# Kernel tuning notes

Measured on AMD Instinct MI355X. Metric: run time of the kernel, lower is better.

The kernel has to match this reference:

```python
import jax, jax.numpy as jnp
import numpy as np

STRIDE = (1, 1)
PADDING = ((1, 1), (1, 1))


def setup_inputs() -> dict:
    key = jax.random.key(0)
    kx, kw, kb = jax.random.split(key, 3)
    x = jax.random.normal(kx, (32, 128, 56, 56), dtype=jnp.float32)
    weight = jax.random.normal(kw, (256, 128, 3, 3), dtype=jnp.float32)  # (O, I, kh, kw)
    bias = jax.random.normal(kb, (256,), dtype=jnp.float32)
    return {"x": x, "weight": weight, "bias": bias}


def reference(x, weight, bias):
    # Faithful dense 2D convolution (cross-correlation, as in the torch module),
    # NCHW input, OIHW weight, stride 1, padding 1.
    out = jax.lax.conv_general_dilated(
        x, weight,
        window_strides=STRIDE,
        padding=PADDING,
        dimension_numbers=("NCHW", "OIHW", "NCHW"),
    )
    return out + bias[None, :, None, None]
```

## Files before the change

### kernel.cpp

```cpp
#include <hip/hip_runtime.h>

#define C_IN   128
#define H_IN   56
#define W_IN   56
#define HW     3136
#define CHW    401408
#define O_OUT  256
#define OHW    802816

#define LDK 72
#define XTP 132

typedef __bf16 bf16x8 __attribute__((ext_vector_type(8)));
typedef float  f32x4  __attribute__((ext_vector_type(4)));
typedef unsigned short ushort_t;
typedef ushort_t ushort8 __attribute__((ext_vector_type(8)));

__device__ __forceinline__ ushort_t f2bf(float f) {
    union { float f; unsigned u; } v; v.f = f;
    unsigned r = (v.u + 0x7fffu + ((v.u >> 16) & 1u)) >> 16;
    return (ushort_t)r;
}

typedef const __attribute__((address_space(1))) unsigned int* gas_ptr;
typedef __attribute__((address_space(3))) unsigned int* las_ptr;
__device__ __forceinline__ void gl_lds16(const void* g, void* l) {
    __builtin_amdgcn_global_load_lds((gas_ptr)g, (las_ptr)l, 16, 0, 0);
}


__global__ void wt2_kernel(const float* __restrict__ w, ushort_t* __restrict__ wbf) {
    int idx = blockIdx.x * 256 + threadIdx.x;
    if (idx >= 9 * 256 * 128) return;
    int pos = idx >> 15;
    int rem = idx & 32767;
    int o   = rem >> 7;
    int c   = rem & 127;
    int s    = pos * 2 + (c >> 6);
    int slot = ((c >> 3) & 7) ^ (o & 7);
    wbf[((s * 256 + o) << 6) + (slot << 3) + (c & 7)] = f2bf(w[o * 1152 + c * 9 + pos]);
}

__global__ __launch_bounds__(256)
void xt2_kernel(const float* __restrict__ x, ushort_t* __restrict__ xbp) {
    const int b  = blockIdx.x;
    const int n  = b / 58;
    const int hp = b - n * 58;
    ushort_t* orow = xbp + (size_t)(n * 58 + hp) * 7424;
    const int t = threadIdx.x;
    ushort8 z = ushort8{0,0,0,0,0,0,0,0};

    if (hp == 0 || hp == 57) {
        #pragma unroll
        for (int i = 0; i < 4; ++i) {
            int u = i * 256 + t;
            if (u < 928) *(ushort8*)(orow + u * 8) = z;
        }
        return;
    }

    __shared__ ushort_t T[56 * XTP];
    const int h = hp - 1;
    const float* src = x + (size_t)n * CHW + h * W_IN;
    #pragma unroll
    for (int i = 0; i < 7; ++i) {
        int g  = i * 256 + t;
        int c  = g / 14;
        int f4 = g - c * 14;
        f32x4 v = *(const f32x4*)(src + (size_t)c * HW + f4 * 4);
        #pragma unroll
        for (int j = 0; j < 4; ++j)
            T[(f4 * 4 + j) * XTP + c] = f2bf(v[j]);
    }
    __syncthreads();
    #pragma unroll
    for (int i = 0; i < 4; ++i) {
        int u = i * 256 + t;
        if (u < 928) {
            int wp = u >> 4, gg = u & 15;
            ushort8 v = (wp == 0 || wp == 57) ? z
                        : *(const ushort8*)(&T[(wp - 1) * XTP + gg * 8]);
            *(ushort8*)(orow + wp * 128 + ((gg ^ (wp & 7)) << 3)) = v;
        }
    }
}

__global__ __launch_bounds__(256, 3)
void conv12_kernel(const ushort_t* __restrict__ xbp, const ushort_t* __restrict__ wbf,
                   const float* __restrict__ bias, float* __restrict__ out) {
    __shared__ ushort_t As[128 * 64];
    __shared__ ushort_t Bs[128 * 64];

    const int tid  = threadIdx.x;
    const int lane = tid & 63;
    const int wave = tid >> 6;
    const int wm   = wave >> 1;
    const int wn   = wave & 1;
    const int l15  = lane & 15;
    const int quad = lane >> 4;
    const int om   = wm * 64;

    int tau = blockIdx.x;
    tau = (tau & 7) * 196 + (tau >> 3);
    const int pix_base = (tau >> 1) * 128;
    const int ob       = (tau & 1) << 7;

    long Bc[4];
    {
        #pragma unroll
        for (int c = 0; c < 4; ++c) {
            int idx = (wave * 4 + c) * 64 + lane;
            int px  = idx >> 3;
            int j8  = idx & 7;
            int p   = pix_base + px;
            int n_  = p / HW;
            int hw  = p - n_ * HW;
            int h   = hw / W_IN;
            int w_  = hw - h * W_IN;
            Bc[c] = (long)(n_ * 58 + h + 1) * 14848 + (long)(w_ + 1) * 256 + j8 * 16;
        }
    }

    int aoff[4];
    #pragma unroll
    for (int t = 0; t < 4; ++t) {
        int ol = om + t * 16 + l15;
        aoff[t] = ol * 128 + ((quad ^ (ol & 7)) << 4);
    }
    int pxb[4], pr7[4], obo[4];
    #pragma unroll
    for (int u = 0; u < 4; ++u) {
        int pxr = wn * 64 + u * 16 + l15;
        int p   = pix_base + pxr;
        pxb[u]  = pxr * 128;
        pr7[u]  = (p + 1) & 7;
        obo[u]  = p;
    }

    f32x4 acc[4][4];
    #pragma unroll
    for (int t = 0; t < 4; ++t)
        #pragma unroll
        for (int u = 0; u < 4; ++u)
            acc[t][u] = f32x4{0.f, 0.f, 0.f, 0.f};

    const char* xg = (const char*)xbp;
    const char* wg = (const char*)wbf;
    char* AsB = (char*)As;
    char* BsB = (char*)Bs;

    for (int q = 0; q < 18; ++q) {
        const int pos  = q >> 1;
        const int half = q & 1;
        const int dh   = pos / 3 - 1;
        const int dw   = pos - (pos / 3) * 3 - 1;
        const long soff = (long)dh * 14848 + (long)dw * 256 + half * 128;

        {
            const char* as = wg + (size_t)q * 32768 + (size_t)ob * 128;
            #pragma unroll
            for (int j = 0; j < 4; ++j) {
                const int blk = (wave * 4 + j) * 1024;
                gl_lds16(as + blk + (lane << 4), AsB + blk);
                gl_lds16(xg + Bc[j] + soff,      BsB + blk);
            }
        }
        __syncthreads();

        int boff[4];
        #pragma unroll
        for (int u = 0; u < 4; ++u) {
            const int key = (pr7[u] + dw + 8) & 7;
            boff[u] = pxb[u] + ((quad ^ key) << 4);
        }
        #pragma unroll
        for (int ks = 0; ks < 2; ++ks) {
            const int kx = ks << 6;
            bf16x8 af[4], bf[4];
            #pragma unroll
            for (int t = 0; t < 4; ++t)
                af[t] = *(const bf16x8*)(AsB + (aoff[t] ^ kx));
            #pragma unroll
            for (int u = 0; u < 4; ++u)
                bf[u] = *(const bf16x8*)(BsB + (boff[u] ^ kx));
            #pragma unroll
            for (int t = 0; t < 4; ++t)
                #pragma unroll
                for (int u = 0; u < 4; ++u)
                    acc[t][u] = __builtin_amdgcn_mfma_f32_16x16x32_bf16(
                                    af[t], bf[u], acc[t][u], 0, 0, 0);
        }
        __syncthreads();
    }

    #pragma unroll
    for (int u = 0; u < 4; ++u) {
        const int pp  = obo[u];
        const int nn  = pp / HW;
        const int hw2 = pp - nn * HW;
        const long obase = (long)nn * OHW + hw2;
        #pragma unroll
        for (int t = 0; t < 4; ++t) {
            const int o_base = ob + wm * 64 + t * 16 + quad * 4;
            #pragma unroll
            for (int r = 0; r < 4; ++r) {
                const int o = o_base + r;
                out[obase + (long)o * HW] = acc[t][u][r] + bias[o];
            }
        }
    }
}


__global__ void wt_kernel(const float* __restrict__ w, ushort_t* __restrict__ wbf) {
    int idx = blockIdx.x * 256 + threadIdx.x;
    if (idx >= 9 * 256 * 128) return;
    int pos = idx >> 15;
    int rem = idx & 32767;
    int o   = rem >> 7;
    int c   = rem & 127;
    wbf[idx] = f2bf(w[o * 1152 + c * 9 + pos]);
}

__global__ __launch_bounds__(512, 4)
void conv_kernel(const float* __restrict__ x, const ushort_t* __restrict__ wbf,
                 const float* __restrict__ bias, float* __restrict__ out) {
    __shared__ ushort_t As[256 * LDK];
    __shared__ ushort_t Bs[128 * LDK];

    const int tid  = threadIdx.x;
    const int lane = tid & 63;
    const int wave = tid >> 6;
    const int wm   = wave >> 1;
    const int wn   = wave & 1;
    const int l15  = lane & 15;
    const int quad = lane >> 4;

    const int pix_base = blockIdx.x * 128;
    const int px  = tid & 127;
    const int cg0 = tid >> 7;
    const int p   = pix_base + px;
    const int n_img = p / HW;
    const int hw    = p - n_img * HW;
    const int h     = hw / W_IN;
    const int w_    = hw - h * W_IN;
    const float* ximg = x + (long)n_img * CHW;

    f32x4 acc[4][4];
    #pragma unroll
    for (int t = 0; t < 4; ++t)
        #pragma unroll
        for (int u = 0; u < 4; ++u)
            acc[t][u] = f32x4{0.f, 0.f, 0.f, 0.f};

    for (int pos = 0; pos < 9; ++pos) {
        const int dh = pos / 3 - 1;
        const int dw = pos - (pos / 3) * 3 - 1;
        const int ih = h + dh;
        const int iw = w_ + dw;
        const bool valid = ((unsigned)ih < (unsigned)H_IN) && ((unsigned)iw < (unsigned)W_IN);
        const float* xsrc = ximg + ih * W_IN + iw;

        for (int half = 0; half < 2; ++half) {
            const int c0 = half * 64;
            {
                const ushort_t* wsrc = wbf + ((pos * 256) << 7) + c0;
                #pragma unroll
                for (int sj = 0; sj < 4; ++sj) {
                    const int o  = (tid >> 3) + sj * 64;
                    const int cg = tid & 7;
                    ushort8 v = *(const ushort8*)(wsrc + (o << 7) + cg * 8);
                    *(ushort8*)(&As[o * LDK + cg * 8]) = v;
                }
            }
            {
                #pragma unroll
                for (int sj = 0; sj < 2; ++sj) {
                    const int cg = cg0 + sj * 4;
                    const float* src = xsrc + (long)(c0 + cg * 8) * HW;
                    ushort8 v;
                    #pragma unroll
                    for (int j = 0; j < 8; ++j) {
                        float f = valid ? src[j * HW] : 0.0f;
                        v[j] = f2bf(f);
                    }
                    *(ushort8*)(&Bs[px * LDK + cg * 8]) = v;
                }
            }
            __syncthreads();

            #pragma unroll
            for (int ks = 0; ks < 2; ++ks) {
                bf16x8 af[4], bfv[4];
                #pragma unroll
                for (int t = 0; t < 4; ++t) {
                    const int row = wm * 64 + t * 16 + l15;
                    af[t] = *(const bf16x8*)(&As[row * LDK + ks * 32 + quad * 8]);
                }
                #pragma unroll
                for (int u = 0; u < 4; ++u) {
                    const int col = wn * 64 + u * 16 + l15;
                    bfv[u] = *(const bf16x8*)(&Bs[col * LDK + ks * 32 + quad * 8]);
                }
                #pragma unroll
                for (int t = 0; t < 4; ++t)
                    #pragma unroll
                    for (int u = 0; u < 4; ++u)
                        acc[t][u] = __builtin_amdgcn_mfma_f32_16x16x32_bf16(af[t], bfv[u], acc[t][u], 0, 0, 0);
            }
            __syncthreads();
        }
    }

    #pragma unroll
    for (int u = 0; u < 4; ++u) {
        const int col = wn * 64 + u * 16 + l15;
        const int pp  = pix_base + col;
        const int hw2 = pp - (pp / HW) * HW;
        const long obase = (long)(pp / HW) * OHW + hw2;
        #pragma unroll
        for (int t = 0; t < 4; ++t) {
            const int o_base = wm * 64 + t * 16 + quad * 4;
            #pragma unroll
            for (int r = 0; r < 4; ++r) {
                const int o = o_base + r;
                out[obase + (long)o * HW] = acc[t][u][r] + bias[o];
            }
        }
    }
}

extern "C" void kernel_launch(void* const* d_in, const int* in_sizes, int n_in,
                              void* d_out, int out_size, void* d_ws, size_t ws_size,
                              hipStream_t stream) {
    const float* x    = (const float*)d_in[0];
    const float* w    = (const float*)d_in[1];
    const float* bias = (const float*)d_in[2];
    float* out        = (float*)d_out;

    const size_t NEED_NEW = 589824u + 27557888u;

    if (ws_size >= NEED_NEW) {
        ushort_t* wbf = (ushort_t*)d_ws;
        ushort_t* xbp = (ushort_t*)((char*)d_ws + 589824);
        hipLaunchKernelGGL(wt2_kernel, dim3(1152), dim3(256), 0, stream, w, wbf);
        hipLaunchKernelGGL(xt2_kernel, dim3(1856), dim3(256), 0, stream, x, xbp);
        hipLaunchKernelGGL(conv12_kernel, dim3(1568), dim3(256), 0, stream,
                           xbp, wbf, bias, out);
    } else {
        ushort_t* wbf = (ushort_t*)d_ws;
        hipLaunchKernelGGL(wt_kernel, dim3(1152), dim3(256), 0, stream, w, wbf);
        hipLaunchKernelGGL(conv_kernel, dim3(100352 / 128), dim3(512), 0, stream,
                           x, wbf, bias, out);
    }
}
```

Baseline: 209.6 us.

## Triple-buffer LDS with 32-wide K steps and full 256-channel output tiles

```diff
diff --git a/kernel.cpp b/kernel.cpp
--- a/kernel.cpp
+++ b/kernel.cpp
@@ -29,20 +29,24 @@
 }
 
 
-__global__ void wt2_kernel(const float* __restrict__ w, ushort_t* __restrict__ wbf) {
+__global__ void wt5_kernel(const float* __restrict__ w, ushort_t* __restrict__ wbf) {
     int idx = blockIdx.x * 256 + threadIdx.x;
-    if (idx >= 9 * 256 * 128) return;
-    int pos = idx >> 15;
-    int rem = idx & 32767;
-    int o   = rem >> 7;
-    int c   = rem & 127;
-    int s    = pos * 2 + (c >> 6);
-    int slot = ((c >> 3) & 7) ^ (o & 7);
-    wbf[((s * 256 + o) << 6) + (slot << 3) + (c & 7)] = f2bf(w[o * 1152 + c * 9 + pos]);
+    if (idx >= 294912) return;
+    int v  = idx >> 13;
+    int r  = idx & 8191;
+    int o  = r >> 5;
+    int s  = r & 31;
+    int j2 = s >> 3;
+    int e  = s & 7;
+    int a   = v & 3;
+    int pos = v >> 2;
+    int g2 = j2 ^ ((o >> 1) & 3);
+    int c  = a * 32 + g2 * 8 + e;
+    wbf[idx] = f2bf(w[o * 1152 + c * 9 + pos]);
 }
 
 __global__ __launch_bounds__(256)
-void xt2_kernel(const float* __restrict__ x, ushort_t* __restrict__ xbp) {
+void xt3_kernel(const float* __restrict__ x, ushort_t* __restrict__ xbp) {
     const int b  = blockIdx.x;
     const int n  = b / 58;
     const int hp = b - n * 58;
@@ -80,16 +84,19 @@
             int wp = u >> 4, gg = u & 15;
             ushort8 v = (wp == 0 || wp == 57) ? z
                         : *(const ushort8*)(&T[(wp - 1) * XTP + gg * 8]);
-            *(ushort8*)(orow + wp * 128 + ((gg ^ (wp & 7)) << 3)) = v;
-        }
-    }
-}
-
-__global__ __launch_bounds__(256, 3)
-void conv12_kernel(const ushort_t* __restrict__ xbp, const ushort_t* __restrict__ wbf,
+            const int a  = gg >> 2;
+            const int g2 = gg & 3;
+            const int k  = (wp & 3) ^ ((wp >> 2) & 3);
+            *(ushort8*)(orow + wp * 128 + ((a * 4 + (g2 ^ k)) << 3)) = v;
+        }
+    }
+}
+
+__global__ __launch_bounds__(512, 4)
+void conv13_kernel(const ushort_t* __restrict__ xbp, const ushort_t* __restrict__ wbf,
                    const float* __restrict__ bias, float* __restrict__ out) {
-    __shared__ ushort_t As[128 * 64];
-    __shared__ ushort_t Bs[128 * 64];
+    __shared__ ushort_t Alds[3][8192];
+    __shared__ ushort_t Blds[3][4096];
 
     const int tid  = threadIdx.x;
     const int lane = tid & 63;
@@ -98,43 +105,42 @@
     const int wn   = wave & 1;
     const int l15  = lane & 15;
     const int quad = lane >> 4;
-    const int om   = wm * 64;
-
-    int tau = blockIdx.x;
-    tau = (tau & 7) * 196 + (tau >> 3);
-    const int pix_base = (tau >> 1) * 128;
-    const int ob       = (tau & 1) << 7;
-
-    long Bc[4];
+    const int wb10 = wave << 10;
+
+    int b = blockIdx.x;
+    b = (b & 7) * 98 + (b >> 3);
+    const int pix_base = b * 128;
+
+    int aoff[4];
+    #pragma unroll
+    for (int t = 0; t < 4; ++t) {
+        int o = wm * 64 + t * 16 + l15;
+        aoff[t] = o * 64 + ((quad ^ ((o >> 1) & 3)) << 4);
+    }
+
+    int pxb[4], w1[4];
+    #pragma unroll
+    for (int u = 0; u < 4; ++u) {
+        int px = wn * 64 + u * 16 + l15;
+        int p  = pix_base + px;
+        int n_ = p / HW;
+        int hw = p - n_ * HW;
+        int h  = hw / W_IN;
+        int w_ = hw - h * W_IN;
+        pxb[u] = px * 64;
+        w1[u]  = w_ + 1;
+    }
+
+    int Brow;
     {
-        #pragma unroll
-        for (int c = 0; c < 4; ++c) {
-            int idx = (wave * 4 + c) * 64 + lane;
-            int px  = idx >> 3;
-            int j8  = idx & 7;
-            int p   = pix_base + px;
-            int n_  = p / HW;
-            int hw  = p - n_ * HW;
-            int h   = hw / W_IN;
-            int w_  = hw - h * W_IN;
-            Bc[c] = (long)(n_ * 58 + h + 1) * 14848 + (long)(w_ + 1) * 256 + j8 * 16;
-        }
-    }
-
-    int aoff[4];
-    #pragma unroll
-    for (int t = 0; t < 4; ++t) {
-        int ol = om + t * 16 + l15;
-        aoff[t] = ol * 128 + ((quad ^ (ol & 7)) << 4);
-    }
-    int pxb[4], pr7[4], obo[4];
-    #pragma unroll
-    for (int u = 0; u < 4; ++u) {
-        int pxr = wn * 64 + u * 16 + l15;
-        int p   = pix_base + pxr;
-        pxb[u]  = pxr * 128;
-        pr7[u]  = (p + 1) & 7;
-        obo[u]  = p;
+        int spx = tid >> 2;
+        int j2  = tid & 3;
+        int sp  = pix_base + spx;
+        int sn  = sp / HW;
+        int shw = sp - sn * HW;
+        int sh  = shw / W_IN;
+        int sw  = shw - sh * W_IN;
+        Brow = ((sn * 58 + sh + 1) * 58 + (sw + 1)) * 256 + j2 * 16;
     }
 
     f32x4 acc[4][4];
@@ -144,69 +150,84 @@
         for (int u = 0; u < 4; ++u)
             acc[t][u] = f32x4{0.f, 0.f, 0.f, 0.f};
 
-    const char* xg = (const char*)xbp;
-    const char* wg = (const char*)wbf;
-    char* AsB = (char*)As;
-    char* BsB = (char*)Bs;
-
-    for (int q = 0; q < 18; ++q) {
-        const int pos  = q >> 1;
-        const int half = q & 1;
-        const int dh   = pos / 3 - 1;
-        const int dw   = pos - (pos / 3) * 3 - 1;
-        const long soff = (long)dh * 14848 + (long)dw * 256 + half * 128;
-
-        {
-            const char* as = wg + (size_t)q * 32768 + (size_t)ob * 128;
-            #pragma unroll
-            for (int j = 0; j < 4; ++j) {
-                const int blk = (wave * 4 + j) * 1024;
-                gl_lds16(as + blk + (lane << 4), AsB + blk);
-                gl_lds16(xg + Bc[j] + soff,      BsB + blk);
-            }
-        }
-        __syncthreads();
-
-        int boff[4];
+    const char* wgb = (const char*)wbf;
+    const char* xgb = (const char*)xbp;
+
+    char* A0 = (char*)Alds[0]; char* A1 = (char*)Alds[1]; char* A2 = (char*)Alds[2];
+    char* B0 = (char*)Blds[0]; char* B1 = (char*)Blds[1]; char* B2 = (char*)Blds[2];
+
+#define ISSUE(vv, Ad, Bd) { \
+    const int v_ = (vv); \
+    const int pos_ = v_ >> 2, a_ = v_ & 3; \
+    const int dh_ = pos_ / 3 - 1; \
+    const int dw_ = pos_ - (pos_ / 3) * 3 - 1; \
+    const char* as_ = wgb + (size_t)v_ * 16384; \
+    gl_lds16(as_ + wb10 + (lane << 4),        (Ad) + wb10); \
+    gl_lds16(as_ + 8192 + wb10 + (lane << 4), (Ad) + 8192 + wb10); \
+    const int soff_ = (dh_ * 58 + dw_) * 256 + a_ * 64; \
+    gl_lds16(xgb + (long)(Brow + soff_),      (Bd) + wb10); }
+
+    ISSUE(0, A0, B0);
+    ISSUE(1, A1, B1);
+    asm volatile("s_waitcnt vmcnt(3)" ::: "memory");
+    __builtin_amdgcn_s_barrier();
+
+    for (int q = 0; q < 36; ++q) {
+        const int pos = q >> 2;
+        const int dw  = pos - (pos / 3) * 3 - 1;
+
+        bf16x8 af[4], bf[4];
+        #pragma unroll
+        for (int t = 0; t < 4; ++t)
+            af[t] = *(const bf16x8*)(A0 + aoff[t]);
         #pragma unroll
         for (int u = 0; u < 4; ++u) {
-            const int key = (pr7[u] + dw + 8) & 7;
-            boff[u] = pxb[u] + ((quad ^ key) << 4);
-        }
-        #pragma unroll
-        for (int ks = 0; ks < 2; ++ks) {
-            const int kx = ks << 6;
-            bf16x8 af[4], bf[4];
-            #pragma unroll
-            for (int t = 0; t < 4; ++t)
-                af[t] = *(const bf16x8*)(AsB + (aoff[t] ^ kx));
+            const int ww  = w1[u] + dw;
+            const int key = (ww & 3) ^ ((ww >> 2) & 3);
+            bf[u] = *(const bf16x8*)(B0 + pxb[u] + ((quad ^ key) << 4));
+        }
+
+        if (q < 34) ISSUE(q + 2, A2, B2);
+
+        __builtin_amdgcn_s_barrier();
+        asm volatile("s_waitcnt lgkmcnt(0)" ::: "memory");
+        __builtin_amdgcn_sched_barrier(0);
+        __builtin_amdgcn_s_setprio(1);
+        #pragma unroll
+        for (int t = 0; t < 4; ++t)
             #pragma unroll
             for (int u = 0; u < 4; ++u)
-                bf[u] = *(const bf16x8*)(BsB + (boff[u] ^ kx));
+                acc[t][u] = __builtin_amdgcn_mfma_f32_16x16x32_bf16(
+                                af[t], bf[u], acc[t][u], 0, 0, 0);
+        __builtin_amdgcn_s_setprio(0);
+        __builtin_amdgcn_sched_barrier(0);
+
+        if (q < 34) asm volatile("s_waitcnt vmcnt(3)" ::: "memory");
+        else        asm volatile("s_waitcnt vmcnt(0)" ::: "memory");
+        __builtin_amdgcn_s_barrier();
+
+        char* tA = A0; A0 = A1; A1 = A2; A2 = tA;
+        char* tB = B0; B0 = B1; B1 = B2; B2 = tB;
+    }
+#undef ISSUE
+
+    f32x4 bv[4];
+    #pragma unroll
+    for (int t = 0; t < 4; ++t)
+        bv[t] = *(const f32x4*)(bias + wm * 64 + t * 16 + quad * 4);
+    #pragma unroll
+    for (int u = 0; u < 4; ++u) {
+        const int px  = wn * 64 + u * 16 + l15;
+        const int p   = pix_base + px;
+        const int nn  = p / HW;
+        const int hw2 = p - nn * HW;
+        float* op = out + (size_t)nn * OHW + hw2;
+        #pragma unroll
+        for (int t = 0; t < 4; ++t) {
+            const int o0 = wm * 64 + t * 16 + quad * 4;
             #pragma unroll
-            for (int t = 0; t < 4; ++t)
-                #pragma unroll
-                for (int u = 0; u < 4; ++u)
-                    acc[t][u] = __builtin_amdgcn_mfma_f32_16x16x32_bf16(
-                                    af[t], bf[u], acc[t][u], 0, 0, 0);
-        }
-        __syncthreads();
-    }
-
-    #pragma unroll
-    for (int u = 0; u < 4; ++u) {
-        const int pp  = obo[u];
-        const int nn  = pp / HW;
-        const int hw2 = pp - nn * HW;
-        const long obase = (long)nn * OHW + hw2;
-        #pragma unroll
-        for (int t = 0; t < 4; ++t) {
-            const int o_base = ob + wm * 64 + t * 16 + quad * 4;
-            #pragma unroll
-            for (int r = 0; r < 4; ++r) {
-                const int o = o_base + r;
-                out[obase + (long)o * HW] = acc[t][u][r] + bias[o];
-            }
+            for (int r = 0; r < 4; ++r)
+                op[(size_t)(o0 + r) * HW] = acc[t][u][r] + bv[t][r];
         }
     }
 }
@@ -343,9 +364,9 @@
     if (ws_size >= NEED_NEW) {
         ushort_t* wbf = (ushort_t*)d_ws;
         ushort_t* xbp = (ushort_t*)((char*)d_ws + 589824);
-        hipLaunchKernelGGL(wt2_kernel, dim3(1152), dim3(256), 0, stream, w, wbf);
-        hipLaunchKernelGGL(xt2_kernel, dim3(1856), dim3(256), 0, stream, x, xbp);
-        hipLaunchKernelGGL(conv12_kernel, dim3(1568), dim3(256), 0, stream,
+        hipLaunchKernelGGL(wt5_kernel, dim3(1152), dim3(256), 0, stream, w, wbf);
+        hipLaunchKernelGGL(xt3_kernel, dim3(1856), dim3(256), 0, stream, x, xbp);
+        hipLaunchKernelGGL(conv13_kernel, dim3(784), dim3(512), 0, stream,
                            xbp, wbf, bias, out);
     } else {
         ushort_t* wbf = (ushort_t*)d_ws;
```

Result: no change. 210.2 us (+0.3%).
